# Optimization experiments

Hardware: AMD Instinct MI355X
Metric: run time of the kernel (lower is better)

The kernel has to match this reference:

```python
import jax, jax.numpy as jnp
import numpy as np
from jax import lax

WINDOW_SIZE = 11
SIGMA = 1.5
C1 = 0.01 ** 2
C2 = 0.03 ** 2


def _gaussian_window(channel, window_size=WINDOW_SIZE, sigma=SIGMA, dtype=jnp.float32):
    x = jnp.arange(window_size, dtype=dtype) - window_size // 2
    g = jnp.exp(-(x ** 2) / (2.0 * sigma ** 2))
    g = g / g.sum()
    w2 = jnp.outer(g, g)  # [K, K]
    # depthwise kernel: [C_out=C, C_in/groups=1, K, K]
    return jnp.broadcast_to(w2[None, None], (channel, 1, window_size, window_size))


def _dwconv(x, window, channel, window_size=WINDOW_SIZE):
    pad = window_size // 2
    return lax.conv_general_dilated(
        x, window,
        window_strides=(1, 1),
        padding=[(pad, pad), (pad, pad)],
        dimension_numbers=('NCHW', 'OIHW', 'NCHW'),
        feature_group_count=channel,
    )


def setup_inputs() -> dict:
    key = jax.random.key(0)
    k1, k2 = jax.random.split(key)
    img1 = jax.random.uniform(k1, (16, 3, 512, 512), dtype=jnp.float32)
    img2 = jax.random.uniform(k2, (16, 3, 512, 512), dtype=jnp.float32)
    return {"img1": img1, "img2": img2}


def reference(img1, img2):
    channel = img1.shape[1]
    window = _gaussian_window(channel, dtype=img1.dtype)

    mu1 = _dwconv(img1, window, channel)
    mu2 = _dwconv(img2, window, channel)
    mu1_sq = mu1 * mu1
    mu2_sq = mu2 * mu2
    mu1_mu2 = mu1 * mu2

    sigma1_sq = _dwconv(img1 * img1, window, channel) - mu1_sq
    sigma2_sq = _dwconv(img2 * img2, window, channel) - mu2_sq
    sigma12 = _dwconv(img1 * img2, window, channel) - mu1_mu2

    ssim_map = ((2.0 * mu1_mu2 + C1) * (2.0 * sigma12 + C2)) / (
        (mu1_sq + mu2_sq + C1) * (sigma1_sq + sigma2_sq + C2))
    return ssim_map.mean()
```

## Files before the change

kernel.cpp:

```cpp
#include <hip/hip_runtime.h>

namespace {
constexpr int IMG_W = 512, IMG_H = 512;
constexpr int TW = 32, TH = 64;
constexpr int IN_H = TH + 10;
constexpr int IN_UNITS = 22;
constexpr int P1_TASKS = IN_H * IN_UNITS;
constexpr float C1c = 0.01f * 0.01f;
constexpr float C2c = 0.03f * 0.03f;

constexpr float GW[11] = {
    1.0283799e-03f, 7.5987582e-03f, 3.6000773e-02f, 1.0936069e-01f,
    2.1300554e-01f, 2.6601172e-01f, 2.1300554e-01f, 1.0936069e-01f,
    3.6000773e-02f, 7.5987582e-03f, 1.0283799e-03f
};

using v2f = __attribute__((ext_vector_type(2))) float;
using v4f = __attribute__((ext_vector_type(4))) float;

__device__ __forceinline__ void pkfma(v2f& acc, v2f w, v2f a) {
    asm("v_pk_fma_f32 %0, %1, %2, %0" : "+v"(acc) : "s"(w), "v"(a));
}
__device__ __forceinline__ v2f pkmul(v2f a, v2f b) {
    v2f d;
    asm("v_pk_mul_f32 %0, %1, %2" : "=v"(d) : "v"(a), "v"(b));
    return d;
}
__device__ __forceinline__ v2f bcast(float w) { v2f r; r.x = w; r.y = w; return r; }

__device__ __forceinline__ int pidx(int row, int col) {
    return row * 32 + ((col + row) & 31);
}
}

__global__ __launch_bounds__(256, 4) void ssim_tile_kernel(
        const float* __restrict__ img1, const float* __restrict__ img2,
        double* __restrict__ acc)
{
    __shared__ v4f plane[IN_H * 32];
    __shared__ float wred[4];

    const int tid = threadIdx.x;
    const size_t base = (size_t)blockIdx.z * (IMG_W * IMG_H);
    const float* p1 = img1 + base;
    const float* p2 = img2 + base;
    const int x0e = blockIdx.x * TW - 6;
    const int y0  = blockIdx.y * TH - 5;

    {
        int r   = tid / 22;
        int cf2 = tid - r * 22;
        int goff = (y0 + r) * IMG_W + x0e + 2 * cf2;
        const bool interior =
            blockIdx.x > 0 && blockIdx.x < gridDim.x - 1 &&
            blockIdx.y > 0 && blockIdx.y < gridDim.y - 1;
        if (interior) {
#pragma unroll
            for (int i = 0; i < 7; ++i) {
                if (i < 6 || tid < P1_TASKS - 6 * 256) {
                    const float2 a = *(const float2*)&p1[goff];
                    const float2 b = *(const float2*)&p2[goff];
                    v4f q; q.x = a.x; q.y = b.x; q.z = a.y; q.w = b.y;
                    plane[pidx(r, cf2)] = q;
                }
                const bool wrap = cf2 + 14 >= 22;
                cf2  += wrap ? -8 : 14;
                r    += wrap ? 12 : 11;
                goff += wrap ? 12 * IMG_W - 16 : 11 * IMG_W + 28;
            }
        } else {
#pragma unroll
            for (int i = 0; i < 7; ++i) {
                if (i < 6 || tid < P1_TASKS - 6 * 256) {
                    const int gy = y0 + r;
                    const int gx = x0e + 2 * cf2;
                    float a0 = 0.f, a1 = 0.f, b0 = 0.f, b1 = 0.f;
                    if (gy >= 0 && gy < IMG_H) {
                        if (gx >= 0 && gx < IMG_W)         { a0 = p1[goff];     b0 = p2[goff]; }
                        if (gx + 1 >= 0 && gx + 1 < IMG_W) { a1 = p1[goff + 1]; b1 = p2[goff + 1]; }
                    }
                    v4f q; q.x = a0; q.y = b0; q.z = a1; q.w = b1;
                    plane[pidx(r, cf2)] = q;
                }
                const bool wrap = cf2 + 14 >= 22;
                cf2  += wrap ? -8 : 14;
                r    += wrap ? 12 : 11;
                goff += wrap ? 12 * IMG_W - 16 : 11 * IMG_W + 28;
            }
        }
    }
    __syncthreads();

    v2f muA[8], sxA[8], muB[8], sxB[8];
    const int rA = tid >> 2;
    const int gA = tid & 3;
    const bool hasB = tid < 40;
    const int rB = 64 + (tid >> 2);

    auto hconv = [&](int r2, int g2, v2f* mu8, v2f* sx8) {
#pragma unroll
        for (int j = 0; j < 8; ++j) { mu8[j] = bcast(0.f); sx8[j] = bcast(0.f); }
        const int rowb = r2 * 32;
        const int cb   = g2 * 4 + r2;
#pragma unroll
        for (int m = 0; m < 10; ++m) {
            const v4f q = plane[rowb + ((cb + m) & 31)];
#pragma unroll
            for (int half = 0; half < 2; ++half) {
                const int k = 2 * m + half;
                v2f v;
                v.x = half ? q.z : q.x;
                v.y = half ? q.w : q.y;
                const v2f a2 = pkmul(v, v);
                v2f sx;
                sx.x = a2.x + a2.y;
                sx.y = v.x * v.y;
#pragma unroll
                for (int j = 0; j < 8; ++j) {
                    const int t = k - j - 1;
                    if (t >= 0 && t < 11) {
                        const v2f w2 = bcast(GW[t]);
                        pkfma(mu8[j], w2, v);
                        pkfma(sx8[j], w2, sx);
                    }
                }
            }
        }
    };

    hconv(rA, gA, muA, sxA);
    if (hasB) hconv(rB, gA, muB, sxB);
    __syncthreads();
#pragma unroll
    for (int j = 0; j < 8; ++j) {
        v4f q;
        q.x = muA[j].x; q.y = muA[j].y;
        q.z = sxA[j].x; q.w = sxA[j].y;
        plane[pidx(rA, 8 * gA + j)] = q;
    }
    if (hasB) {
#pragma unroll
        for (int j = 0; j < 8; ++j) {
            v4f q;
            q.x = muB[j].x; q.y = muB[j].y;
            q.z = sxB[j].x; q.w = sxB[j].y;
            plane[pidx(rB, 8 * gA + j)] = q;
        }
    }
    __syncthreads();

    const int c3 = tid & 31;
    const int rb = (tid >> 5) * 8;
    v2f mu8[8], sx8[8];
#pragma unroll
    for (int j = 0; j < 8; ++j) { mu8[j] = bcast(0.f); sx8[j] = bcast(0.f); }
#pragma unroll
    for (int k = 0; k < 18; ++k) {
        const v4f q = plane[pidx(rb + k, c3)];
        v2f hm; hm.x = q.x; hm.y = q.y;
        v2f hx; hx.x = q.z; hx.y = q.w;
#pragma unroll
        for (int j = 0; j < 8; ++j) {
            const int t = k - j;
            if (t >= 0 && t < 11) {
                const v2f w2 = bcast(GW[t]);
                pkfma(mu8[j], w2, hm);
                pkfma(sx8[j], w2, hx);
            }
        }
    }
    float lsum = 0.f;
#pragma unroll
    for (int j = 0; j < 8; ++j) {
        const v2f musq = pkmul(mu8[j], mu8[j]);
        const float mu12 = mu8[j].x * mu8[j].y;
        const float sden = musq.x + musq.y;
        const float s12v = sx8[j].y - mu12;
        const float ssum = sx8[j].x - sden;
        const float num = (2.f * mu12 + C1c) * (2.f * s12v + C2c);
        const float den = (sden + C1c) * (ssum + C2c);
        lsum += __fdividef(num, den);
    }

#pragma unroll
    for (int off = 32; off > 0; off >>= 1)
        lsum += __shfl_down(lsum, off, 64);
    if ((tid & 63) == 0) wred[tid >> 6] = lsum;
    __syncthreads();
    if (tid == 0) {
        const int bid = (blockIdx.z * gridDim.y + blockIdx.y) * gridDim.x + blockIdx.x;
        unsafeAtomicAdd(&acc[bid & 255],
                        (double)(wred[0] + wred[1] + wred[2] + wred[3]));
    }
}

__global__ __launch_bounds__(256) void ssim_final_kernel(
        const double* __restrict__ acc, float* __restrict__ out, double inv_total)
{
    const int tid = threadIdx.x;
    double a = acc[tid];
#pragma unroll
    for (int off = 32; off > 0; off >>= 1)
        a += __shfl_down(a, off, 64);
    __shared__ double ws[4];
    if ((tid & 63) == 0) ws[tid >> 6] = a;
    __syncthreads();
    if (tid == 0)
        out[0] = (float)((ws[0] + ws[1] + ws[2] + ws[3]) * inv_total);
}

extern "C" void kernel_launch(void* const* d_in, const int* in_sizes, int n_in,
                              void* d_out, int out_size, void* d_ws, size_t ws_size,
                              hipStream_t stream)
{
    const float* img1 = (const float*)d_in[0];
    const float* img2 = (const float*)d_in[1];
    double* acc = (double*)d_ws;

    hipMemsetAsync(d_ws, 0, 256 * sizeof(double), stream);

    const int nch = in_sizes[0] / (IMG_W * IMG_H);
    dim3 grid(IMG_W / TW, IMG_H / TH, nch);
    ssim_tile_kernel<<<grid, 256, 0, stream>>>(img1, img2, acc);

    const double inv_total = 1.0 / (double)in_sizes[0];
    ssim_final_kernel<<<1, 256, 0, stream>>>(acc, (float*)d_out, inv_total);
}
```

Before: 160.0 us.

## Grow tile block to 384 threads and rebalance horizontal and vertical pass work

Raises the block size from 256 to 384 threads so the horizontal pass gives each of the 296 active threads exactly one row. Previously 40 threads had to process a second row while the rest waited. The vertical pass is split into 12 column groups: four groups produce 6 rows and eight produce 5, via a templated helper. This removes the load imbalance and lowers per-thread register demand, at the cost of more redundant halo reads from shared memory in the vertical pass and some idle threads in the horizontal pass. Occupancy now depends on the larger block and the launch-bound hint of 6 blocks, which the shared memory footprint may not allow.

```diff
diff --git a/kernel.cpp b/kernel.cpp
--- a/kernel.cpp
+++ b/kernel.cpp
@@ -6,6 +6,7 @@
 constexpr int IN_H = TH + 10;
 constexpr int IN_UNITS = 22;
 constexpr int P1_TASKS = IN_H * IN_UNITS;
+constexpr int NTHREADS = 384;
 constexpr float C1c = 0.01f * 0.01f;
 constexpr float C2c = 0.03f * 0.03f;
 
@@ -31,14 +32,49 @@
 __device__ __forceinline__ int pidx(int row, int col) {
     return row * 32 + ((col + row) & 31);
 }
-}
-
-__global__ __launch_bounds__(256, 4) void ssim_tile_kernel(
+
+template<int LEN>
+__device__ __forceinline__ float vconv(const v4f* plane, int rb, int c3) {
+    v2f mu[LEN], sx[LEN];
+#pragma unroll
+    for (int j = 0; j < LEN; ++j) { mu[j] = bcast(0.f); sx[j] = bcast(0.f); }
+#pragma unroll
+    for (int k = 0; k < LEN + 10; ++k) {
+        const v4f q = plane[pidx(rb + k, c3)];
+        v2f hm; hm.x = q.x; hm.y = q.y;
+        v2f hx; hx.x = q.z; hx.y = q.w;
+#pragma unroll
+        for (int j = 0; j < LEN; ++j) {
+            const int t = k - j;
+            if (t >= 0 && t < 11) {
+                const v2f w2 = bcast(GW[t]);
+                pkfma(mu[j], w2, hm);
+                pkfma(sx[j], w2, hx);
+            }
+        }
+    }
+    float lsum = 0.f;
+#pragma unroll
+    for (int j = 0; j < LEN; ++j) {
+        const v2f musq = pkmul(mu[j], mu[j]);
+        const float mu12 = mu[j].x * mu[j].y;
+        const float sden = musq.x + musq.y;
+        const float s12v = sx[j].y - mu12;
+        const float ssum = sx[j].x - sden;
+        const float num = (2.f * mu12 + C1c) * (2.f * s12v + C2c);
+        const float den = (sden + C1c) * (ssum + C2c);
+        lsum += __fdividef(num, den);
+    }
+    return lsum;
+}
+}
+
+__global__ __launch_bounds__(NTHREADS, 6) void ssim_tile_kernel(
         const float* __restrict__ img1, const float* __restrict__ img2,
         double* __restrict__ acc)
 {
     __shared__ v4f plane[IN_H * 32];
-    __shared__ float wred[4];
+    __shared__ float wred[8];
 
     const int tid = threadIdx.x;
     const size_t base = (size_t)blockIdx.z * (IMG_W * IMG_H);
@@ -56,22 +92,22 @@
             blockIdx.y > 0 && blockIdx.y < gridDim.y - 1;
         if (interior) {
 #pragma unroll
-            for (int i = 0; i < 7; ++i) {
-                if (i < 6 || tid < P1_TASKS - 6 * 256) {
+            for (int i = 0; i < 5; ++i) {
+                if (i < 4 || tid < P1_TASKS - 4 * NTHREADS) {
                     const float2 a = *(const float2*)&p1[goff];
                     const float2 b = *(const float2*)&p2[goff];
                     v4f q; q.x = a.x; q.y = b.x; q.z = a.y; q.w = b.y;
                     plane[pidx(r, cf2)] = q;
                 }
-                const bool wrap = cf2 + 14 >= 22;
-                cf2  += wrap ? -8 : 14;
-                r    += wrap ? 12 : 11;
-                goff += wrap ? 12 * IMG_W - 16 : 11 * IMG_W + 28;
+                const bool wrap = cf2 >= 12;
+                cf2  += wrap ? -12 : 10;
+                r    += wrap ? 18 : 17;
+                goff += wrap ? 18 * IMG_W - 24 : 17 * IMG_W + 20;
             }
         } else {
 #pragma unroll
-            for (int i = 0; i < 7; ++i) {
-                if (i < 6 || tid < P1_TASKS - 6 * 256) {
+            for (int i = 0; i < 5; ++i) {
+                if (i < 4 || tid < P1_TASKS - 4 * NTHREADS) {
                     const int gy = y0 + r;
                     const int gx = x0e + 2 * cf2;
                     float a0 = 0.f, a1 = 0.f, b0 = 0.f, b1 = 0.f;
@@ -82,26 +118,24 @@
                     v4f q; q.x = a0; q.y = b0; q.z = a1; q.w = b1;
                     plane[pidx(r, cf2)] = q;
                 }
-                const bool wrap = cf2 + 14 >= 22;
-                cf2  += wrap ? -8 : 14;
-                r    += wrap ? 12 : 11;
-                goff += wrap ? 12 * IMG_W - 16 : 11 * IMG_W + 28;
-            }
-        }
-    }
-    __syncthreads();
-
-    v2f muA[8], sxA[8], muB[8], sxB[8];
+                const bool wrap = cf2 >= 12;
+                cf2  += wrap ? -12 : 10;
+                r    += wrap ? 18 : 17;
+                goff += wrap ? 18 * IMG_W - 24 : 17 * IMG_W + 20;
+            }
+        }
+    }
+    __syncthreads();
+
+    v2f mu8[8], sx8[8];
     const int rA = tid >> 2;
     const int gA = tid & 3;
-    const bool hasB = tid < 40;
-    const int rB = 64 + (tid >> 2);
-
-    auto hconv = [&](int r2, int g2, v2f* mu8, v2f* sx8) {
+    const bool act2 = tid < 296;
+    if (act2) {
 #pragma unroll
         for (int j = 0; j < 8; ++j) { mu8[j] = bcast(0.f); sx8[j] = bcast(0.f); }
-        const int rowb = r2 * 32;
-        const int cb   = g2 * 4 + r2;
+        const int rowb = rA * 32;
+        const int cb   = gA * 4 + rA;
 #pragma unroll
         for (int m = 0; m < 10; ++m) {
             const v4f q = plane[rowb + ((cb + m) & 31)];
@@ -126,61 +160,24 @@
                 }
             }
         }
-    };
-
-    hconv(rA, gA, muA, sxA);
-    if (hasB) hconv(rB, gA, muB, sxB);
-    __syncthreads();
-#pragma unroll
-    for (int j = 0; j < 8; ++j) {
-        v4f q;
-        q.x = muA[j].x; q.y = muA[j].y;
-        q.z = sxA[j].x; q.w = sxA[j].y;
-        plane[pidx(rA, 8 * gA + j)] = q;
-    }
-    if (hasB) {
+    }
+    __syncthreads();
+    if (act2) {
 #pragma unroll
         for (int j = 0; j < 8; ++j) {
             v4f q;
-            q.x = muB[j].x; q.y = muB[j].y;
-            q.z = sxB[j].x; q.w = sxB[j].y;
-            plane[pidx(rB, 8 * gA + j)] = q;
+            q.x = mu8[j].x; q.y = mu8[j].y;
+            q.z = sx8[j].x; q.w = sx8[j].y;
+            plane[pidx(rA, 8 * gA + j)] = q;
         }
     }
     __syncthreads();
 
     const int c3 = tid & 31;
-    const int rb = (tid >> 5) * 8;
-    v2f mu8[8], sx8[8];
-#pragma unroll
-    for (int j = 0; j < 8; ++j) { mu8[j] = bcast(0.f); sx8[j] = bcast(0.f); }
-#pragma unroll
-    for (int k = 0; k < 18; ++k) {
-        const v4f q = plane[pidx(rb + k, c3)];
-        v2f hm; hm.x = q.x; hm.y = q.y;
-        v2f hx; hx.x = q.z; hx.y = q.w;
-#pragma unroll
-        for (int j = 0; j < 8; ++j) {
-            const int t = k - j;
-            if (t >= 0 && t < 11) {
-                const v2f w2 = bcast(GW[t]);
-                pkfma(mu8[j], w2, hm);
-                pkfma(sx8[j], w2, hx);
-            }
-        }
-    }
-    float lsum = 0.f;
-#pragma unroll
-    for (int j = 0; j < 8; ++j) {
-        const v2f musq = pkmul(mu8[j], mu8[j]);
-        const float mu12 = mu8[j].x * mu8[j].y;
-        const float sden = musq.x + musq.y;
-        const float s12v = sx8[j].y - mu12;
-        const float ssum = sx8[j].x - sden;
-        const float num = (2.f * mu12 + C1c) * (2.f * s12v + C2c);
-        const float den = (sden + C1c) * (ssum + C2c);
-        lsum += __fdividef(num, den);
-    }
+    const int gi = tid >> 5;
+    float lsum;
+    if (gi < 4) lsum = vconv<6>(plane, 6 * gi, c3);
+    else        lsum = vconv<5>(plane, 24 + 5 * (gi - 4), c3);
 
 #pragma unroll
     for (int off = 32; off > 0; off >>= 1)
@@ -190,7 +187,8 @@
     if (tid == 0) {
         const int bid = (blockIdx.z * gridDim.y + blockIdx.y) * gridDim.x + blockIdx.x;
         unsafeAtomicAdd(&acc[bid & 255],
-                        (double)(wred[0] + wred[1] + wred[2] + wred[3]));
+                        (double)(wred[0] + wred[1] + wred[2] +
+                                 wred[3] + wred[4] + wred[5]));
     }
 }
 
@@ -221,7 +219,7 @@
 
     const int nch = in_sizes[0] / (IMG_W * IMG_H);
     dim3 grid(IMG_W / TW, IMG_H / TH, nch);
-    ssim_tile_kernel<<<grid, 256, 0, stream>>>(img1, img2, acc);
+    ssim_tile_kernel<<<grid, NTHREADS, 0, stream>>>(img1, img2, acc);
 
     const double inv_total = 1.0 / (double)in_sizes[0];
     ssim_final_kernel<<<1, 256, 0, stream>>>(acc, (float*)d_out, inv_total);
```

Measured after the change: 170.3 us. +6.4%, slower.
